# Performance work log

Hardware: AMD Instinct MI355X
Metric: run time of the kernel (lower is better)

## Reference

```python
import jax, jax.numpy as jnp
import numpy as np

N_HEADS = 8
D_EMBED = 512
D_HEAD = D_EMBED // N_HEADS


def setup_inputs() -> dict:
    key = jax.random.key(0)
    ks = jax.random.split(key, 5)
    s = 1.0 / np.sqrt(D_EMBED)
    return {
        "x": jax.random.normal(ks[0], (2, 4096, D_EMBED), dtype=jnp.float32),
        "in_proj_w": jax.random.normal(ks[1], (3 * D_EMBED, D_EMBED), dtype=jnp.float32) * s,
        "in_proj_b": jax.random.normal(ks[2], (3 * D_EMBED,), dtype=jnp.float32) * s,
        "out_proj_w": jax.random.normal(ks[3], (D_EMBED, D_EMBED), dtype=jnp.float32) * s,
        "out_proj_b": jax.random.normal(ks[4], (D_EMBED,), dtype=jnp.float32) * s,
    }


def reference(x, in_proj_w, in_proj_b, out_proj_w, out_proj_b):
    B, S, D = x.shape
    # in_proj: x @ W^T + b, then chunk into q, k, v
    qkv = jnp.einsum("bsd,ed->bse", x, in_proj_w) + in_proj_b  # [B,S,3D]
    q, k, v = jnp.split(qkv, 3, axis=-1)
    # [B,S,D] -> [B,H,S,dh]
    def heads(t):
        return t.reshape(B, S, N_HEADS, D_HEAD).transpose(0, 2, 1, 3)
    q, k, v = heads(q), heads(k), heads(v)
    scale = 1.0 / np.sqrt(D_HEAD).astype(np.float32)
    scores = jnp.einsum("bhqd,bhkd->bhqk", q, k) * scale  # [B,H,S,S]
    attn = jax.nn.softmax(scores, axis=-1)
    out = jnp.einsum("bhqk,bhkd->bhqd", attn, v)  # [B,H,S,dh]
    out = out.transpose(0, 2, 1, 3).reshape(B, S, D)
    return jnp.einsum("bsd,ed->bse", out, out_proj_w) + out_proj_b
```

## Files before the change

### kernel.cpp

```cpp
#include <hip/hip_runtime.h>
#include <cstdint>
#include <cstddef>

typedef __bf16 bf16x8 __attribute__((ext_vector_type(8)));
typedef float f32x4 __attribute__((ext_vector_type(4)));
typedef float f32x16 __attribute__((ext_vector_type(16)));
typedef unsigned int u32x4 __attribute__((ext_vector_type(4)));
typedef unsigned short u16;
typedef unsigned int u32;

#define S_LEN 4096
#define NH 8
#define DH 64
#define D_EMB 512
#define BATCH 2
#define M_ROWS 8192
#define GK 512
#define QSCALE 0.18033688011112042f

__device__ __forceinline__ u16 f2bf(float f) {
  u32 u = __builtin_bit_cast(u32, f);
  u += 0x7FFFu + ((u >> 16) & 1u);
  return (u16)(u >> 16);
}
__device__ __forceinline__ float bf2f(u16 v) {
  return __builtin_bit_cast(float, (u32)v << 16);
}
__device__ __forceinline__ u32 pk2(float a, float b) {
  union { __bf16 h[2]; u32 w; } u;
  u.h[0] = (__bf16)a;
  u.h[1] = (__bf16)b;
  return u.w;
}
__device__ __forceinline__ float fexp2(float x) {
#if __has_builtin(__builtin_amdgcn_exp2f)
  return __builtin_amdgcn_exp2f(x);
#else
  return __expf(x * 0.6931471805599453f);
#endif
}

#define MFMA32(a, b, c) __builtin_amdgcn_mfma_f32_32x32x16_bf16(a, b, c, 0, 0, 0)

#define GLD_LDS16(gsrc, ldst)                                                        \
  __builtin_amdgcn_global_load_lds(                                                  \
      (const __attribute__((address_space(1))) void*)(gsrc),                         \
      (__attribute__((address_space(3))) void*)(ldst), 16, 0, 0)

__global__ void detect_kernel(const u16* __restrict__ x, int* __restrict__ flag) {
  __shared__ int cnt;
  if (threadIdx.x == 0) cnt = 0;
  __syncthreads();
  int plaus = 0;
  for (int i = threadIdx.x; i < 2048; i += 256) {
    u16 u = x[2 * i];
    int ex = (u >> 7) & 0xFF;
    plaus += (ex >= 100 && ex <= 134) ? 1 : 0;
  }
  atomicAdd(&cnt, plaus);
  __syncthreads();
  if (threadIdx.x == 0) *flag = (cnt > 1024) ? 0 : 1;
}

__global__ void prep_kernel(const void* __restrict__ x, const void* __restrict__ wq,
                            const void* __restrict__ bq, const void* __restrict__ wo,
                            const void* __restrict__ bo,
                            u16* __restrict__ xb, u16* __restrict__ wqb,
                            u16* __restrict__ wob, float* __restrict__ bqf,
                            float* __restrict__ bof, const int* __restrict__ flag) {
  const bool f32 = (*flag != 0);
  const size_t i = (size_t)blockIdx.x * blockDim.x + threadIdx.x;
  if (i < (size_t)M_ROWS * D_EMB)
    xb[i] = f32 ? f2bf(((const float*)x)[i]) : ((const u16*)x)[i];
  if (i < (size_t)3 * D_EMB * D_EMB)
    wqb[i] = f32 ? f2bf(((const float*)wq)[i]) : ((const u16*)wq)[i];
  if (i < (size_t)D_EMB * D_EMB)
    wob[i] = f32 ? f2bf(((const float*)wo)[i]) : ((const u16*)wo)[i];
  if (i < 3 * D_EMB)
    bqf[i] = f32 ? ((const float*)bq)[i] : bf2f(((const u16*)bq)[i]);
  if (i < D_EMB)
    bof[i] = f32 ? ((const float*)bo)[i] : bf2f(((const u16*)bo)[i]);
}

template <int EPI>
__global__ __launch_bounds__(256, 2)
void gemm_bt(const u16* __restrict__ A, const u16* __restrict__ B, int N,
             const float* __restrict__ bias, u16* __restrict__ qout,
             u16* __restrict__ kout, u16* __restrict__ vout, u16* __restrict__ obf,
             float* __restrict__ of32, const int* __restrict__ flag) {
  __shared__ u16 As[128 * 64];
  __shared__ u16 Bs[128 * 64];
  const int tid = threadIdx.x;
  const int wave = tid >> 6, lane = tid & 63;
  const int m0 = blockIdx.x * 128;
  const int n0 = blockIdx.y * 128;
  const int wr = (wave >> 1) * 64, wc = (wave & 1) * 64;

  const int sr = wave * 8 + (lane >> 3);
  const int scb = (lane & 7) * 16;

  f32x4 acc[4][4] = {};

  for (int k0 = 0; k0 < GK; k0 += 64) {
#pragma unroll
    for (int i = 0; i < 4; ++i) {
      const int r = i * 32 + sr;
      const int sc = (scb ^ ((r & 7) << 4)) >> 1;
      GLD_LDS16(A + (size_t)(m0 + r) * GK + k0 + sc, As + i * 2048 + wave * 512);
    }
#pragma unroll
    for (int i = 0; i < 4; ++i) {
      const int r = i * 32 + sr;
      const int sc = (scb ^ ((r & 7) << 4)) >> 1;
      GLD_LDS16(B + (size_t)(n0 + r) * GK + k0 + sc, Bs + i * 2048 + wave * 512);
    }
    __syncthreads();
#pragma unroll
    for (int kk = 0; kk < 2; ++kk) {
      const int cb = kk * 64 + ((lane >> 4) << 4);
      bf16x8 a[4], b[4];
#pragma unroll
      for (int m = 0; m < 4; ++m) {
        const int r = wr + m * 16 + (lane & 15);
        a[m] = *(const bf16x8*)((const char*)As + r * 128 + (cb ^ ((r & 7) << 4)));
      }
#pragma unroll
      for (int n = 0; n < 4; ++n) {
        const int r = wc + n * 16 + (lane & 15);
        b[n] = *(const bf16x8*)((const char*)Bs + r * 128 + (cb ^ ((r & 7) << 4)));
      }
#pragma unroll
      for (int m = 0; m < 4; ++m)
#pragma unroll
        for (int n = 0; n < 4; ++n)
          acc[m][n] = __builtin_amdgcn_mfma_f32_16x16x32_bf16(a[m], b[n], acc[m][n], 0, 0, 0);
    }
    __syncthreads();
  }

  const bool f32out = (EPI == 1) && (*flag != 0);
#pragma unroll
  for (int n = 0; n < 4; ++n) {
    const int col = n0 + wc + n * 16 + (lane & 15);
    const float bv = bias[col];
#pragma unroll
    for (int m = 0; m < 4; ++m) {
#pragma unroll
      for (int r = 0; r < 4; ++r) {
        const int row = m0 + wr + m * 16 + ((lane >> 4) << 2) + r;
        float v = acc[m][n][r] + bv;
        if (EPI == 0) {
          const int bb = row >> 12, s = row & 4095;
          const int which = col >> 9, hc = col & 511;
          const int h = hc >> 6, d = hc & 63;
          const int bh = bb * NH + h;
          if (which == 2) {
            const int t16 = s >> 4, dblk = d >> 5;
            const int lane_ = ((s >> 3) & 1) * 32 + (d & 31);
            const int j = s & 7;
            vout[(((size_t)(bh * 256 + t16) * 2 + dblk) * 64 + lane_) * 8 + j] = f2bf(v);
          } else {
            const int t32 = s >> 5, dk = d >> 4;
            const int lane_ = ((d >> 3) & 1) * 32 + (s & 31);
            const int j = d & 7;
            u16* dst = (which == 0) ? qout : kout;
            const float vv = (which == 0) ? v * QSCALE : v;
            dst[(((size_t)(bh * 128 + t32) * 4 + dk) * 64 + lane_) * 8 + j] = f2bf(vv);
          }
        } else {
          if (f32out)
            of32[(size_t)row * D_EMB + col] = v;
          else
            obf[(size_t)row * D_EMB + col] = f2bf(v);
        }
      }
    }
  }
}

__global__ __launch_bounds__(256, 2)
void flash_attn(const u16* __restrict__ qfrag, const u16* __restrict__ kfrag,
                const u16* __restrict__ vfrag, u16* __restrict__ ao) {
  const int phys = blockIdx.x;
  const int xcd = phys & 7, slot = phys >> 3;
  const int bh = xcd * 2 + (slot >> 5);
  const int qb = slot & 31;
  const int b = bh >> 3, h = bh & 7;

  const int lane = threadIdx.x & 63;
  const int wave = threadIdx.x >> 6;
  const int l31 = lane & 31, hi = lane >> 5;
  const int q0 = qb * 128 + wave * 32;

  bf16x8 qf[4];
  {
    const u16* qb_ = qfrag + ((size_t)(bh * 128 + (q0 >> 5)) * 4) * 512 + lane * 8;
#pragma unroll
    for (int dk = 0; dk < 4; ++dk) qf[dk] = *(const bf16x8*)(qb_ + dk * 512);
  }

  const u16* kb_ = kfrag + (size_t)bh * (128 * 4 * 512) + lane * 8;
  const u16* vb_ = vfrag + (size_t)bh * (256 * 2 * 512) + lane * 8;

  f32x16 accO0 = {}, accO1 = {};
  float m = -1e30f, lst = 0.f;

#pragma unroll 1
  for (int kv0 = 0; kv0 < S_LEN; kv0 += 64) {
    const int t32 = kv0 >> 5, t16 = kv0 >> 4;
    bf16x8 kf0[4], kf1[4], vf0[4], vf1[4];
#pragma unroll
    for (int dk = 0; dk < 4; ++dk) {
      kf0[dk] = *(const bf16x8*)(kb_ + (size_t)(t32 * 4 + dk) * 512);
      kf1[dk] = *(const bf16x8*)(kb_ + (size_t)((t32 + 1) * 4 + dk) * 512);
    }
#pragma unroll
    for (int i = 0; i < 4; ++i) {
      vf0[i] = *(const bf16x8*)(vb_ + (size_t)((t16 + i) * 2 + 0) * 512);
      vf1[i] = *(const bf16x8*)(vb_ + (size_t)((t16 + i) * 2 + 1) * 512);
    }

    f32x16 s0 = {}, s1 = {};
#pragma unroll
    for (int dk = 0; dk < 4; ++dk) {
      s0 = MFMA32(kf0[dk], qf[dk], s0);
      s1 = MFMA32(kf1[dk], qf[dk], s1);
    }

    float mx16[16];
#pragma unroll
    for (int i = 0; i < 16; ++i) mx16[i] = fmaxf(s0[i], s1[i]);
    float mx8[8];
#pragma unroll
    for (int i = 0; i < 8; ++i) mx8[i] = fmaxf(mx16[i], mx16[i + 8]);
    float mx4[4];
#pragma unroll
    for (int i = 0; i < 4; ++i) mx4[i] = fmaxf(mx8[i], mx8[i + 4]);
    const float mown = fmaxf(fmaxf(mx4[0], mx4[1]), fmaxf(mx4[2], mx4[3]));
    const float pf = fmaxf(mown, __shfl_xor(mown, 32, 64));

    if (!__all(pf - m <= 8.0f)) {
      const float mn = fmaxf(m, pf);
      const float alpha = fexp2(m - mn);
      m = mn;
      lst *= alpha;
#pragma unroll
      for (int r = 0; r < 16; ++r) {
        const int qrow = (r & 3) + 8 * (r >> 2) + 4 * hi;
        const float ar = __shfl(alpha, qrow, 64);
        accO0[r] *= ar;
        accO1[r] *= ar;
      }
    }

#pragma unroll
    for (int i = 0; i < 16; ++i) {
      s0[i] = fexp2(s0[i] - m);
      s1[i] = fexp2(s1[i] - m);
    }
    float sm16[16];
#pragma unroll
    for (int i = 0; i < 16; ++i) sm16[i] = s0[i] + s1[i];
    float sm8[8];
#pragma unroll
    for (int i = 0; i < 8; ++i) sm8[i] = sm16[i] + sm16[i + 8];
    float sm4[4];
#pragma unroll
    for (int i = 0; i < 4; ++i) sm4[i] = sm8[i] + sm8[i + 4];
    const float sown = (sm4[0] + sm4[1]) + (sm4[2] + sm4[3]);
    lst += sown + __shfl_xor(sown, 32, 64);

    u32 W0, W1, W2, W3;
#define PACK8(P, B0)                                                   \
    {                                                                  \
      const u32 w0 = pk2(P[B0 + 0], P[B0 + 1]);                        \
      const u32 w1 = pk2(P[B0 + 2], P[B0 + 3]);                        \
      const u32 w2 = pk2(P[B0 + 4], P[B0 + 5]);                        \
      const u32 w3 = pk2(P[B0 + 6], P[B0 + 7]);                        \
      const u32 rA = (u32)__shfl_xor((int)(hi ? w0 : w2), 32, 64);     \
      const u32 rB = (u32)__shfl_xor((int)(hi ? w1 : w3), 32, 64);     \
      W0 = hi ? rA : w0;                                               \
      W1 = hi ? rB : w1;                                               \
      W2 = hi ? w2 : rA;                                               \
      W3 = hi ? w3 : rB;                                               \
    }

    bf16x8 pa;
    PACK8(s0, 0);
    pa = __builtin_bit_cast(bf16x8, (u32x4){W0, W1, W2, W3});
    accO0 = MFMA32(pa, vf0[0], accO0);
    accO1 = MFMA32(pa, vf1[0], accO1);
    PACK8(s0, 8);
    pa = __builtin_bit_cast(bf16x8, (u32x4){W0, W1, W2, W3});
    accO0 = MFMA32(pa, vf0[1], accO0);
    accO1 = MFMA32(pa, vf1[1], accO1);
    PACK8(s1, 0);
    pa = __builtin_bit_cast(bf16x8, (u32x4){W0, W1, W2, W3});
    accO0 = MFMA32(pa, vf0[2], accO0);
    accO1 = MFMA32(pa, vf1[2], accO1);
    PACK8(s1, 8);
    pa = __builtin_bit_cast(bf16x8, (u32x4){W0, W1, W2, W3});
    accO0 = MFMA32(pa, vf0[3], accO0);
    accO1 = MFMA32(pa, vf1[3], accO1);
#undef PACK8
  }

  const float linv = 1.f / lst;
#pragma unroll
  for (int r = 0; r < 16; ++r) {
    const int qrow = (r & 3) + 8 * (r >> 2) + 4 * hi;
    const float li = __shfl(linv, qrow, 64);
    u16* orow = ao + (size_t)(b * S_LEN + q0 + qrow) * D_EMB + h * DH;
    orow[l31] = f2bf(accO0[r] * li);
    orow[32 + l31] = f2bf(accO1[r] * li);
  }
}

extern "C" void kernel_launch(void* const* d_in, const int* in_sizes, int n_in,
                              void* d_out, int out_size, void* d_ws, size_t ws_size,
                              hipStream_t stream) {
  char* w = (char*)d_ws;
  int* flag = (int*)w;
  u16* xb = (u16*)(w + 256);
  u16* wqb = (u16*)(w + 8388864);
  u16* wob = (u16*)(w + 9961728);
  float* bqf = (float*)(w + 10486016);
  float* bof = (float*)(w + 10492160);
  u16* qfr = (u16*)(w + 10494208);
  u16* kfr = (u16*)(w + 18882816);
  u16* vfr = (u16*)(w + 27271424);
  u16* ao = (u16*)(w + 35660032);

  detect_kernel<<<1, 256, 0, stream>>>((const u16*)d_in[0], flag);
  prep_kernel<<<16384, 256, 0, stream>>>(d_in[0], d_in[1], d_in[2], d_in[3], d_in[4],
                                         xb, wqb, wob, bqf, bof, flag);
  gemm_bt<0><<<dim3(64, 12), 256, 0, stream>>>(xb, wqb, 3 * D_EMB, bqf, qfr, kfr, vfr,
                                               nullptr, nullptr, flag);
  flash_attn<<<512, 256, 0, stream>>>(qfr, kfr, vfr, ao);
  gemm_bt<1><<<dim3(64, 4), 256, 0, stream>>>(ao, wob, D_EMB, bof, nullptr, nullptr,
                                              nullptr, (u16*)d_out, (float*)d_out, flag);
}
```

Before: 168.5 us.

## Split flash attention KV range across two wave groups and merge via LDS

Each block now runs 8 waves: two groups of four process the same 128 query rows over different halves of the KV sequence. Their partial softmax states are combined through shared memory using the max/sum rescaling. This doubles the waves per block to raise occupancy and shortens each wave's serial loop, which helps hide latency. It costs extra LDS traffic, two barriers and an extra merge pass. s_setprio hints are also wrapped around the MFMA sequences to favour matrix issue.

```diff
diff --git a/kernel.cpp b/kernel.cpp
--- a/kernel.cpp
+++ b/kernel.cpp
@@ -178,9 +178,12 @@
   }
 }
 
-__global__ __launch_bounds__(256, 2)
+__global__ __launch_bounds__(512, 4)
 void flash_attn(const u16* __restrict__ qfrag, const u16* __restrict__ kfrag,
                 const u16* __restrict__ vfrag, u16* __restrict__ ao) {
+  __shared__ float Ols[4][32][65];
+  __shared__ float Mls[4][2][32][2];
+
   const int phys = blockIdx.x;
   const int xcd = phys & 7, slot = phys >> 3;
   const int bh = xcd * 2 + (slot >> 5);
@@ -189,8 +192,9 @@
 
   const int lane = threadIdx.x & 63;
   const int wave = threadIdx.x >> 6;
+  const int g = wave & 3, hf = wave >> 2;
   const int l31 = lane & 31, hi = lane >> 5;
-  const int q0 = qb * 128 + wave * 32;
+  const int q0 = qb * 128 + g * 32;
 
   bf16x8 qf[4];
   {
@@ -205,8 +209,11 @@
   f32x16 accO0 = {}, accO1 = {};
   float m = -1e30f, lst = 0.f;
 
+  const int kvbeg = hf * (S_LEN / 2);
+  const int kvend = kvbeg + (S_LEN / 2);
+
 #pragma unroll 1
-  for (int kv0 = 0; kv0 < S_LEN; kv0 += 64) {
+  for (int kv0 = kvbeg; kv0 < kvend; kv0 += 64) {
     const int t32 = kv0 >> 5, t16 = kv0 >> 4;
     bf16x8 kf0[4], kf1[4], vf0[4], vf1[4];
 #pragma unroll
@@ -221,11 +228,13 @@
     }
 
     f32x16 s0 = {}, s1 = {};
+    __builtin_amdgcn_s_setprio(1);
 #pragma unroll
     for (int dk = 0; dk < 4; ++dk) {
       s0 = MFMA32(kf0[dk], qf[dk], s0);
       s1 = MFMA32(kf1[dk], qf[dk], s1);
     }
+    __builtin_amdgcn_s_setprio(0);
 
     float mx16[16];
 #pragma unroll
@@ -288,31 +297,63 @@
     bf16x8 pa;
     PACK8(s0, 0);
     pa = __builtin_bit_cast(bf16x8, (u32x4){W0, W1, W2, W3});
+    __builtin_amdgcn_s_setprio(1);
     accO0 = MFMA32(pa, vf0[0], accO0);
     accO1 = MFMA32(pa, vf1[0], accO1);
+    __builtin_amdgcn_s_setprio(0);
     PACK8(s0, 8);
     pa = __builtin_bit_cast(bf16x8, (u32x4){W0, W1, W2, W3});
+    __builtin_amdgcn_s_setprio(1);
     accO0 = MFMA32(pa, vf0[1], accO0);
     accO1 = MFMA32(pa, vf1[1], accO1);
+    __builtin_amdgcn_s_setprio(0);
     PACK8(s1, 0);
     pa = __builtin_bit_cast(bf16x8, (u32x4){W0, W1, W2, W3});
+    __builtin_amdgcn_s_setprio(1);
     accO0 = MFMA32(pa, vf0[2], accO0);
     accO1 = MFMA32(pa, vf1[2], accO1);
+    __builtin_amdgcn_s_setprio(0);
     PACK8(s1, 8);
     pa = __builtin_bit_cast(bf16x8, (u32x4){W0, W1, W2, W3});
+    __builtin_amdgcn_s_setprio(1);
     accO0 = MFMA32(pa, vf0[3], accO0);
     accO1 = MFMA32(pa, vf1[3], accO1);
+    __builtin_amdgcn_s_setprio(0);
 #undef PACK8
   }
 
-  const float linv = 1.f / lst;
-#pragma unroll
-  for (int r = 0; r < 16; ++r) {
-    const int qrow = (r & 3) + 8 * (r >> 2) + 4 * hi;
-    const float li = __shfl(linv, qrow, 64);
-    u16* orow = ao + (size_t)(b * S_LEN + q0 + qrow) * D_EMB + h * DH;
-    orow[l31] = f2bf(accO0[r] * li);
-    orow[32 + l31] = f2bf(accO1[r] * li);
+  if (hi == 0) {
+    Mls[g][hf][l31][0] = m;
+    Mls[g][hf][l31][1] = lst;
+  }
+  __syncthreads();
+  const float mo = Mls[g][1 - hf][l31][0];
+  const float lo = Mls[g][1 - hf][l31][1];
+  const float M = fmaxf(m, mo);
+  const float L = lst * fexp2(m - M) + lo * fexp2(mo - M);
+  const float myw = fexp2(m - M) / L;
+
+  if (hf == 1) {
+#pragma unroll
+    for (int r = 0; r < 16; ++r) {
+      const int qrow = (r & 3) + 8 * (r >> 2) + 4 * hi;
+      const float wr_ = __shfl(myw, qrow, 64);
+      Ols[g][qrow][l31] = accO0[r] * wr_;
+      Ols[g][qrow][32 + l31] = accO1[r] * wr_;
+    }
+  }
+  __syncthreads();
+  if (hf == 0) {
+#pragma unroll
+    for (int r = 0; r < 16; ++r) {
+      const int qrow = (r & 3) + 8 * (r >> 2) + 4 * hi;
+      const float wr_ = __shfl(myw, qrow, 64);
+      const float o0 = accO0[r] * wr_ + Ols[g][qrow][l31];
+      const float o1 = accO1[r] * wr_ + Ols[g][qrow][32 + l31];
+      u16* orow = ao + (size_t)(b * S_LEN + q0 + qrow) * D_EMB + h * DH;
+      orow[l31] = f2bf(o0);
+      orow[32 + l31] = f2bf(o1);
+    }
   }
 }
 
@@ -336,7 +377,7 @@
                                          xb, wqb, wob, bqf, bof, flag);
   gemm_bt<0><<<dim3(64, 12), 256, 0, stream>>>(xb, wqb, 3 * D_EMB, bqf, qfr, kfr, vfr,
                                                nullptr, nullptr, flag);
-  flash_attn<<<512, 256, 0, stream>>>(qfr, kfr, vfr, ao);
+  flash_attn<<<512, 512, 0, stream>>>(qfr, kfr, vfr, ao);
   gemm_bt<1><<<dim3(64, 4), 256, 0, stream>>>(ao, wob, D_EMB, bof, nullptr, nullptr,
                                               nullptr, (u16*)d_out, (float*)d_out, flag);
 }
```

Measured after the change: 273.7 us. 1.62x slower.

## Split flash attention KV range across two blocks and merge partials

Applied to the files above, without the earlier changes.

Splits each query block's KV sweep into two halves processed by separate blocks (1024 blocks instead of 512). Each half writes unnormalized bf16 partial outputs plus running max and sum, and a new merge kernel combines them into the final attention output. The inner loop step shrinks from 64 to 32 keys and launch bounds rise to 4 blocks per CU to increase occupancy. The cost is an extra kernel launch, extra partial-output traffic, and bf16 rounding of the unnormalized partials.

```diff
diff --git a/kernel.cpp b/kernel.cpp
--- a/kernel.cpp
+++ b/kernel.cpp
@@ -7,6 +7,7 @@
 typedef float f32x16 __attribute__((ext_vector_type(16)));
 typedef unsigned int u32x4 __attribute__((ext_vector_type(4)));
 typedef unsigned short u16;
+typedef unsigned short u16x8 __attribute__((ext_vector_type(8)));
 typedef unsigned int u32;
 
 #define S_LEN 4096
@@ -178,14 +179,16 @@
   }
 }
 
-__global__ __launch_bounds__(256, 2)
+__global__ __launch_bounds__(256, 4)
 void flash_attn(const u16* __restrict__ qfrag, const u16* __restrict__ kfrag,
-                const u16* __restrict__ vfrag, u16* __restrict__ ao) {
+                const u16* __restrict__ vfrag, u16* __restrict__ op0,
+                u16* __restrict__ op1, float* __restrict__ ml) {
   const int phys = blockIdx.x;
   const int xcd = phys & 7, slot = phys >> 3;
-  const int bh = xcd * 2 + (slot >> 5);
-  const int qb = slot & 31;
-  const int b = bh >> 3, h = bh & 7;
+  const int bh = xcd * 2 + (slot >> 6);
+  const int rem = slot & 63;
+  const int qb = rem >> 1;
+  const int hf = rem & 1;
 
   const int lane = threadIdx.x & 63;
   const int wave = threadIdx.x >> 6;
@@ -205,34 +208,28 @@
   f32x16 accO0 = {}, accO1 = {};
   float m = -1e30f, lst = 0.f;
 
+  const int kvbeg = hf * (S_LEN / 2);
+  const int kvend = kvbeg + (S_LEN / 2);
+
 #pragma unroll 1
-  for (int kv0 = 0; kv0 < S_LEN; kv0 += 64) {
+  for (int kv0 = kvbeg; kv0 < kvend; kv0 += 32) {
     const int t32 = kv0 >> 5, t16 = kv0 >> 4;
-    bf16x8 kf0[4], kf1[4], vf0[4], vf1[4];
-#pragma unroll
-    for (int dk = 0; dk < 4; ++dk) {
-      kf0[dk] = *(const bf16x8*)(kb_ + (size_t)(t32 * 4 + dk) * 512);
-      kf1[dk] = *(const bf16x8*)(kb_ + (size_t)((t32 + 1) * 4 + dk) * 512);
-    }
-#pragma unroll
-    for (int i = 0; i < 4; ++i) {
-      vf0[i] = *(const bf16x8*)(vb_ + (size_t)((t16 + i) * 2 + 0) * 512);
-      vf1[i] = *(const bf16x8*)(vb_ + (size_t)((t16 + i) * 2 + 1) * 512);
-    }
-
-    f32x16 s0 = {}, s1 = {};
-#pragma unroll
-    for (int dk = 0; dk < 4; ++dk) {
-      s0 = MFMA32(kf0[dk], qf[dk], s0);
-      s1 = MFMA32(kf1[dk], qf[dk], s1);
-    }
-
-    float mx16[16];
-#pragma unroll
-    for (int i = 0; i < 16; ++i) mx16[i] = fmaxf(s0[i], s1[i]);
+    bf16x8 kf[4], vfA[2], vfB[2];
+#pragma unroll
+    for (int dk = 0; dk < 4; ++dk)
+      kf[dk] = *(const bf16x8*)(kb_ + (size_t)(t32 * 4 + dk) * 512);
+    vfA[0] = *(const bf16x8*)(vb_ + (size_t)((t16 + 0) * 2 + 0) * 512);
+    vfB[0] = *(const bf16x8*)(vb_ + (size_t)((t16 + 0) * 2 + 1) * 512);
+    vfA[1] = *(const bf16x8*)(vb_ + (size_t)((t16 + 1) * 2 + 0) * 512);
+    vfB[1] = *(const bf16x8*)(vb_ + (size_t)((t16 + 1) * 2 + 1) * 512);
+
+    f32x16 s = {};
+#pragma unroll
+    for (int dk = 0; dk < 4; ++dk) s = MFMA32(kf[dk], qf[dk], s);
+
     float mx8[8];
 #pragma unroll
-    for (int i = 0; i < 8; ++i) mx8[i] = fmaxf(mx16[i], mx16[i + 8]);
+    for (int i = 0; i < 8; ++i) mx8[i] = fmaxf(s[i], s[i + 8]);
     float mx4[4];
 #pragma unroll
     for (int i = 0; i < 4; ++i) mx4[i] = fmaxf(mx8[i], mx8[i + 4]);
@@ -254,16 +251,10 @@
     }
 
 #pragma unroll
-    for (int i = 0; i < 16; ++i) {
-      s0[i] = fexp2(s0[i] - m);
-      s1[i] = fexp2(s1[i] - m);
-    }
-    float sm16[16];
-#pragma unroll
-    for (int i = 0; i < 16; ++i) sm16[i] = s0[i] + s1[i];
+    for (int i = 0; i < 16; ++i) s[i] = fexp2(s[i] - m);
     float sm8[8];
 #pragma unroll
-    for (int i = 0; i < 8; ++i) sm8[i] = sm16[i] + sm16[i + 8];
+    for (int i = 0; i < 8; ++i) sm8[i] = s[i] + s[i + 8];
     float sm4[4];
 #pragma unroll
     for (int i = 0; i < 4; ++i) sm4[i] = sm8[i] + sm8[i + 4];
@@ -286,34 +277,53 @@
     }
 
     bf16x8 pa;
-    PACK8(s0, 0);
+    PACK8(s, 0);
     pa = __builtin_bit_cast(bf16x8, (u32x4){W0, W1, W2, W3});
-    accO0 = MFMA32(pa, vf0[0], accO0);
-    accO1 = MFMA32(pa, vf1[0], accO1);
-    PACK8(s0, 8);
+    accO0 = MFMA32(pa, vfA[0], accO0);
+    accO1 = MFMA32(pa, vfB[0], accO1);
+    PACK8(s, 8);
     pa = __builtin_bit_cast(bf16x8, (u32x4){W0, W1, W2, W3});
-    accO0 = MFMA32(pa, vf0[1], accO0);
-    accO1 = MFMA32(pa, vf1[1], accO1);
-    PACK8(s1, 0);
-    pa = __builtin_bit_cast(bf16x8, (u32x4){W0, W1, W2, W3});
-    accO0 = MFMA32(pa, vf0[2], accO0);
-    accO1 = MFMA32(pa, vf1[2], accO1);
-    PACK8(s1, 8);
-    pa = __builtin_bit_cast(bf16x8, (u32x4){W0, W1, W2, W3});
-    accO0 = MFMA32(pa, vf0[3], accO0);
-    accO1 = MFMA32(pa, vf1[3], accO1);
+    accO0 = MFMA32(pa, vfA[1], accO0);
+    accO1 = MFMA32(pa, vfB[1], accO1);
 #undef PACK8
   }
 
-  const float linv = 1.f / lst;
+  u16* op = hf ? op1 : op0;
 #pragma unroll
   for (int r = 0; r < 16; ++r) {
     const int qrow = (r & 3) + 8 * (r >> 2) + 4 * hi;
-    const float li = __shfl(linv, qrow, 64);
-    u16* orow = ao + (size_t)(b * S_LEN + q0 + qrow) * D_EMB + h * DH;
-    orow[l31] = f2bf(accO0[r] * li);
-    orow[32 + l31] = f2bf(accO1[r] * li);
-  }
+    const size_t R = (size_t)bh * S_LEN + q0 + qrow;
+    op[R * 64 + l31] = f2bf(accO0[r]);
+    op[R * 64 + 32 + l31] = f2bf(accO1[r]);
+  }
+  if (hi == 0) {
+    const size_t R = (size_t)bh * S_LEN + q0 + l31;
+    ml[((size_t)hf * 65536 + R) * 2 + 0] = m;
+    ml[((size_t)hf * 65536 + R) * 2 + 1] = lst;
+  }
+}
+
+__global__ __launch_bounds__(256)
+void merge_kernel(const u16* __restrict__ op0, const u16* __restrict__ op1,
+                  const float* __restrict__ ml, u16* __restrict__ ao) {
+  const int idx = blockIdx.x * 256 + threadIdx.x;
+  const int R = idx >> 3;
+  const int dd = (idx & 7) * 8;
+  const float m0 = ml[(size_t)R * 2 + 0], l0 = ml[(size_t)R * 2 + 1];
+  const float m1 = ml[((size_t)65536 + R) * 2 + 0], l1 = ml[((size_t)65536 + R) * 2 + 1];
+  const float M = fmaxf(m0, m1);
+  float w0 = fexp2(m0 - M), w1 = fexp2(m1 - M);
+  const float rL = 1.f / (l0 * w0 + l1 * w1);
+  w0 *= rL;
+  w1 *= rL;
+  const u16x8 a = *(const u16x8*)(op0 + (size_t)R * 64 + dd);
+  const u16x8 c = *(const u16x8*)(op1 + (size_t)R * 64 + dd);
+  u16x8 o;
+#pragma unroll
+  for (int j = 0; j < 8; ++j) o[j] = f2bf(bf2f(a[j]) * w0 + bf2f(c[j]) * w1);
+  const int bh = R >> 12, s = R & 4095;
+  const int b = bh >> 3, h = bh & 7;
+  *(u16x8*)(ao + ((size_t)(b * S_LEN + s) * D_EMB + h * DH + dd)) = o;
 }
 
 extern "C" void kernel_launch(void* const* d_in, const int* in_sizes, int n_in,
@@ -330,13 +340,17 @@
   u16* kfr = (u16*)(w + 18882816);
   u16* vfr = (u16*)(w + 27271424);
   u16* ao = (u16*)(w + 35660032);
+  u16* op1 = (u16*)(w + 44048640);
+  u16* op0 = xb;
+  float* ml = (float*)wqb;
 
   detect_kernel<<<1, 256, 0, stream>>>((const u16*)d_in[0], flag);
   prep_kernel<<<16384, 256, 0, stream>>>(d_in[0], d_in[1], d_in[2], d_in[3], d_in[4],
                                          xb, wqb, wob, bqf, bof, flag);
   gemm_bt<0><<<dim3(64, 12), 256, 0, stream>>>(xb, wqb, 3 * D_EMB, bqf, qfr, kfr, vfr,
                                                nullptr, nullptr, flag);
-  flash_attn<<<512, 256, 0, stream>>>(qfr, kfr, vfr, ao);
+  flash_attn<<<1024, 256, 0, stream>>>(qfr, kfr, vfr, op0, op1, ml);
+  merge_kernel<<<2048, 256, 0, stream>>>(op0, op1, ml, ao);
   gemm_bt<1><<<dim3(64, 4), 256, 0, stream>>>(ao, wob, D_EMB, bof, nullptr, nullptr,
                                               nullptr, (u16*)d_out, (float*)d_out, flag);
 }
```

After: 160.4 us. -4.8%, faster.
